# Optimization experiments

Hardware: AMD Instinct MI355X
Metric: run time of the kernel (lower is better)

Reference implementation:

```python
import jax, jax.numpy as jnp
import numpy as np

NUM_ANCHORS = 2
NUM_CLASSES = 20
H = 7
W = 7
IMG_H = 448
IMG_W = 448
NMS_THRESH = 0.7
SCORE_THRESH = 0.05
NBOX = H * W * NUM_ANCHORS  # 98 candidate boxes per image


def _format_outputs(x):
    # x: [b, H*W*(num_anchors*5 + num_classes)] -> decoded boxes/objectness/scores
    b = x.shape[0]
    x = x.reshape(b, H, W, NUM_ANCHORS * 5 + NUM_CLASSES)
    # class scores shared across anchors of a cell (repeat_interleave in torch)
    b_scores = jnp.broadcast_to(
        x[..., -NUM_CLASSES:].reshape(b, H * W, 1, NUM_CLASSES),
        (b, H * W, NUM_ANCHORS, NUM_CLASSES),
    )
    xa = x[..., : NUM_ANCHORS * 5].reshape(b, H, W, NUM_ANCHORS, 5)
    c_x = jnp.arange(W, dtype=x.dtype) * (IMG_W / W)
    c_y = jnp.arange(H, dtype=x.dtype) * (IMG_H / H)
    b_x = jax.nn.sigmoid(xa[..., 0]) + c_x[None, None, :, None]
    b_y = jax.nn.sigmoid(xa[..., 1]) + c_y[None, :, None, None]
    b_w = jax.nn.sigmoid(xa[..., 2])
    b_h = jax.nn.sigmoid(xa[..., 3])
    b_coords = jnp.stack((b_x, b_y, b_w, b_h), axis=-1).reshape(b, H * W, NUM_ANCHORS, 4)
    b_o = jax.nn.sigmoid(xa[..., 4]).reshape(b, H * W, NUM_ANCHORS)
    return b_coords, b_o, b_scores


def _pairwise_iou(boxes):
    # boxes: [n, 4] xyxy -> [n, n] IoU (torchvision box_iou semantics, 0 where union==0)
    area = (boxes[:, 2] - boxes[:, 0]) * (boxes[:, 3] - boxes[:, 1])
    lt = jnp.maximum(boxes[:, None, :2], boxes[None, :, :2])
    rb = jnp.minimum(boxes[:, None, 2:], boxes[None, :, 2:])
    wh = jnp.clip(rb - lt, 0.0)
    inter = wh[..., 0] * wh[..., 1]
    union = area[:, None] + area[None, :] - inter
    return jnp.where(union > 0, inter / union, 0.0)


def _per_image(coords, o, sc):
    # coords: [NBOX,4] (x,y,w,h), o: [NBOX], sc: [NBOX,NUM_CLASSES]
    valid = o >= 0.5  # objectness gate (b_o >= 0.5 selection in torch)
    labels = jnp.argmax(sc, axis=-1)
    scores = jnp.max(sc, axis=-1)
    # xywh -> xyxy, clamp to [0,1] (as in post_process)
    boxes = jnp.clip(
        jnp.concatenate([coords[:, :2], coords[:, :2] + coords[:, 2:]], axis=-1), 0.0, 1.0
    )
    # sort by score descending, invalid boxes pushed to the end
    s = jnp.where(valid, scores, -jnp.inf)
    order = jnp.argsort(-s)
    boxes_s = boxes[order]
    scores_s = scores[order]
    labels_s = labels[order]
    valid_s = valid[order]
    iou = _pairwise_iou(boxes_s)
    idxs = jnp.arange(NBOX)

    def body(i, alive):
        # if box i is still alive, suppress later boxes with IoU > thresh
        suppress = (iou[i] > NMS_THRESH) & (idxs > i) & alive[i]
        return alive & ~suppress

    alive = jax.lax.fori_loop(0, NBOX, body, valid_s)
    keep = alive & (scores_s >= SCORE_THRESH)
    boxes_out = jnp.where(keep[:, None], boxes_s, 0.0)
    scores_out = jnp.where(keep, scores_s, 0.0)
    labels_out = jnp.where(keep, labels_s, 0)
    return boxes_out, scores_out, labels_out, keep


def setup_inputs() -> dict:
    key = jax.random.key(0)
    x = jax.random.normal(key, (8192, H * W * (NUM_ANCHORS * 5 + NUM_CLASSES)), dtype=jnp.float32)
    return {"x": x}


def reference(x):
    b_coords, b_o, b_scores = _format_outputs(x)
    b = x.shape[0]
    coords = b_coords.reshape(b, -1, 4)
    o = b_o.reshape(b, -1)
    sc = b_scores.reshape(b, -1, NUM_CLASSES)
    boxes, scores, labels, keep = jax.vmap(_per_image)(coords, o, sc)
    # padded detections: [b, NBOX, 4], [b, NBOX], [b, NBOX], keep mask [b, NBOX]
    return boxes, scores, labels, keep
```

## Files before the change

kernel.cpp:

```cpp
#include <hip/hip_runtime.h>
#include <math.h>

#define NBOX 98
#define ROWLEN 1470
#define NMS_T 0.7f
#define SCORE_T 0.05f

__device__ __forceinline__ float sigm(float v) {
    return 1.0f / (1.0f + expf(-v));
}

__global__ __launch_bounds__(128) void yolo_post(const float* __restrict__ x,
                                                 float* __restrict__ out,
                                                 int batch) {
    const int b    = blockIdx.x;
    const int tid  = threadIdx.x;
    const int wid  = tid >> 6;
    const int lane = tid & 63;

    __shared__ float  row[ROWLEN];
    __shared__ float  cscore[NBOX];
    __shared__ float4 sbox[NBOX];
    __shared__ float  sarea[NBOX];
    __shared__ float  ssc[NBOX];
    __shared__ int    slab[NBOX];
    __shared__ unsigned long long m0[NBOX], m1[NBOX];
    __shared__ unsigned long long aliveW[2];
    __shared__ int    sCnt[2];

    const float2* xr2 = reinterpret_cast<const float2*>(x + (size_t)b * ROWLEN);
    float2* row2 = reinterpret_cast<float2*>(row);
    for (int i = tid; i < ROWLEN / 2; i += 128) row2[i] = xr2[i];
    __syncthreads();

    float4 box = make_float4(0.f, 0.f, 0.f, 0.f);
    float  mx  = 0.f;
    int    ml  = 0;
    bool   valid = false;
    if (tid < NBOX) {
        const int k  = tid >> 1;
        const int a  = tid & 1;
        const int ci = k / 7;
        const int cj = k - ci * 7;
        const float* p = row + k * 30 + a * 5;
        const float bx = sigm(p[0]) + (float)cj * 64.0f;
        const float by = sigm(p[1]) + (float)ci * 64.0f;
        const float bw = sigm(p[2]);
        const float bh = sigm(p[3]);
        valid = (p[4] >= 0.0f);

        const float* c = row + k * 30 + 10;
        mx = c[0]; ml = 0;
        #pragma unroll
        for (int t = 1; t < 20; ++t) {
            float v = c[t];
            if (v > mx) { mx = v; ml = t; }
        }
        box.x = fminf(fmaxf(bx, 0.f), 1.f);
        box.y = fminf(fmaxf(by, 0.f), 1.f);
        box.z = fminf(fmaxf(bx + bw, 0.f), 1.f);
        box.w = fminf(fmaxf(by + bh, 0.f), 1.f);
    }

    const unsigned long long bal = __ballot(valid);
    if (lane == 0) sCnt[wid] = (int)__popcll(bal);
    __syncthreads();
    const int V = sCnt[0] + sCnt[1];
    const int c = (int)__popcll(bal & ((1ull << lane) - 1ull)) + (wid ? sCnt[0] : 0);
    if (valid) cscore[c] = mx;
    __syncthreads();

    if (valid) {
        int rank = 0;
        for (int j = 0; j < V; ++j) {
            const float kj = cscore[j];
            rank += (kj > mx) || ((kj == mx) && (j < c));
        }
        sbox[rank]  = box;
        sarea[rank] = (box.z - box.x) * (box.w - box.y);
        ssc[rank]   = mx;
        slab[rank]  = ml;
    }
    __syncthreads();

    if (tid < V) {
        const float4 bi = sbox[tid];
        const float  ai = sarea[tid];
        unsigned long long mm0 = 0ull, mm1 = 0ull;
        const int e0 = (V < 64) ? V : 64;
        unsigned long long bit = 1ull;
        for (int j = 0; j < e0; ++j, bit <<= 1) {
            const float4 bj = sbox[j];
            const float w = fmaxf(fminf(bi.z, bj.z) - fmaxf(bi.x, bj.x), 0.f);
            const float h = fmaxf(fminf(bi.w, bj.w) - fmaxf(bi.y, bj.y), 0.f);
            const float inter = w * h;
            const float uni = (ai + sarea[j]) - inter;
            if (uni > 0.f && inter > NMS_T * uni) mm0 |= bit;
        }
        if (V > 64) {
            bit = 1ull;
            for (int j = 64; j < V; ++j, bit <<= 1) {
                const float4 bj = sbox[j];
                const float w = fmaxf(fminf(bi.z, bj.z) - fmaxf(bi.x, bj.x), 0.f);
                const float h = fmaxf(fminf(bi.w, bj.w) - fmaxf(bi.y, bj.y), 0.f);
                const float inter = w * h;
                const float uni = (ai + sarea[j]) - inter;
                if (uni > 0.f && inter > NMS_T * uni) mm1 |= bit;
            }
        }
        if (tid < 64) {
            mm0 &= ~((2ull << tid) - 1ull);
        } else {
            mm0 = 0ull;
            mm1 &= ~((2ull << (tid - 64)) - 1ull);
        }
        m0[tid] = mm0;
        m1[tid] = mm1;
    }
    __syncthreads();

    if (tid == 0) {
        if (V <= 64) {
            unsigned long long a0 = (V == 64) ? ~0ull : ((1ull << V) - 1ull);
            for (int i = 0; i < V; ++i)
                if ((a0 >> i) & 1ull) a0 &= ~m0[i];
            aliveW[0] = a0; aliveW[1] = 0ull;
        } else {
            unsigned long long a0 = ~0ull;
            unsigned long long a1 = (1ull << (V - 64)) - 1ull;
            for (int i = 0; i < 64; ++i)
                if ((a0 >> i) & 1ull) { a0 &= ~m0[i]; a1 &= ~m1[i]; }
            for (int i = 64; i < V; ++i)
                if ((a1 >> (i - 64)) & 1ull) a1 &= ~m1[i];
            aliveW[0] = a0; aliveW[1] = a1;
        }
    }
    __syncthreads();

    if (tid < NBOX) {
        float4 bo = make_float4(0.f, 0.f, 0.f, 0.f);
        float so = 0.f, lo = 0.f, ko = 0.f;
        if (tid < V) {
            const bool al = (tid < 64) ? ((aliveW[0] >> tid) & 1ull)
                                       : ((aliveW[1] >> (tid - 64)) & 1ull);
            const float s = ssc[tid];
            if (al && s >= SCORE_T) {
                bo = sbox[tid]; so = s; lo = (float)slab[tid]; ko = 1.0f;
            }
        }
        *reinterpret_cast<float4*>(out + (size_t)b * (NBOX * 4) + (size_t)tid * 4) = bo;
        const size_t base1 = (size_t)batch * (NBOX * 4);
        const size_t bn    = (size_t)batch * NBOX;
        out[base1 +          (size_t)b * NBOX + tid] = so;
        out[base1 + bn +     (size_t)b * NBOX + tid] = lo;
        out[base1 + 2 * bn + (size_t)b * NBOX + tid] = ko;
    }
}

extern "C" void kernel_launch(void* const* d_in, const int* in_sizes, int n_in,
                              void* d_out, int out_size, void* d_ws, size_t ws_size,
                              hipStream_t stream) {
    const float* x = (const float*)d_in[0];
    float* out = (float*)d_out;
    const int batch = in_sizes[0] / ROWLEN;
    yolo_post<<<batch, 128, 0, stream>>>(x, out, batch);
}
```

Baseline: 118.2 us.

## Split IoU mask work across both waves and alias shared buffers

The pairwise IoU matrix is now split by column half across the two waves. Previously wave 1 sat mostly idle while wave 0's threads looped over all V boxes. Each wave writes a partial suppression mask that is ORed during a now-branchless serial NMS scan. The shared-memory arrays for the sorted boxes, scores, areas and labels now alias the input row buffer to shrink LDS use, and the row load loop is unrolled. The trade-offs are doubled mask storage, extra OR work in the serial scan, and reliance on barrier ordering to keep the aliasing safe.

```diff
diff --git a/kernel.cpp b/kernel.cpp
--- a/kernel.cpp
+++ b/kernel.cpp
@@ -18,24 +18,29 @@
     const int wid  = tid >> 6;
     const int lane = tid & 63;
 
-    __shared__ float  row[ROWLEN];
-    __shared__ float  cscore[NBOX];
-    __shared__ float4 sbox[NBOX];
-    __shared__ float  sarea[NBOX];
-    __shared__ float  ssc[NBOX];
-    __shared__ int    slab[NBOX];
-    __shared__ unsigned long long m0[NBOX], m1[NBOX];
+    __shared__ __align__(16) char ubuf[ROWLEN * 4];
+    __shared__ unsigned long long m0h[2 * NBOX], m1h[2 * NBOX];
     __shared__ unsigned long long aliveW[2];
-    __shared__ int    sCnt[2];
+    __shared__ int sCnt[2];
+
+    float*  row    = reinterpret_cast<float*>(ubuf);
+    float4* sbox   = reinterpret_cast<float4*>(ubuf);
+    float*  cscore = reinterpret_cast<float*>(ubuf + 1568);
+    float*  sarea  = reinterpret_cast<float*>(ubuf + 1960);
+    float*  ssc    = reinterpret_cast<float*>(ubuf + 2352);
+    float*  slabf  = reinterpret_cast<float*>(ubuf + 2744);
 
     const float2* xr2 = reinterpret_cast<const float2*>(x + (size_t)b * ROWLEN);
     float2* row2 = reinterpret_cast<float2*>(row);
-    for (int i = tid; i < ROWLEN / 2; i += 128) row2[i] = xr2[i];
+    #pragma unroll
+    for (int i = 0; i < 6; ++i) {
+        const int idx = tid + i * 128;
+        if (idx < ROWLEN / 2) row2[idx] = xr2[idx];
+    }
     __syncthreads();
 
     float4 box = make_float4(0.f, 0.f, 0.f, 0.f);
-    float  mx  = 0.f;
-    int    ml  = 0;
+    float  mx  = 0.f, mlf = 0.f;
     bool   valid = false;
     if (tid < NBOX) {
         const int k  = tid >> 1;
@@ -49,13 +54,14 @@
         const float bh = sigm(p[3]);
         valid = (p[4] >= 0.0f);
 
-        const float* c = row + k * 30 + 10;
-        mx = c[0]; ml = 0;
+        const float* cc = row + k * 30 + 10;
+        mx = cc[0]; int ml = 0;
         #pragma unroll
         for (int t = 1; t < 20; ++t) {
-            float v = c[t];
+            const float v = cc[t];
             if (v > mx) { mx = v; ml = t; }
         }
+        mlf = (float)ml;
         box.x = fminf(fmaxf(bx, 0.f), 1.f);
         box.y = fminf(fmaxf(by, 0.f), 1.f);
         box.z = fminf(fmaxf(bx + bw, 0.f), 1.f);
@@ -79,61 +85,67 @@
         sbox[rank]  = box;
         sarea[rank] = (box.z - box.x) * (box.w - box.y);
         ssc[rank]   = mx;
-        slab[rank]  = ml;
+        slabf[rank] = mlf;
     }
     __syncthreads();
 
-    if (tid < V) {
-        const float4 bi = sbox[tid];
-        const float  ai = sarea[tid];
+    const int Vh  = (V + 1) >> 1;
+    const int jlo = wid ? Vh : 0;
+    const int jhi = wid ? V  : Vh;
+
+    auto iou_row = [&](int i) {
+        const float4 bi = sbox[i];
+        const float  ai = sarea[i];
         unsigned long long mm0 = 0ull, mm1 = 0ull;
-        const int e0 = (V < 64) ? V : 64;
-        unsigned long long bit = 1ull;
-        for (int j = 0; j < e0; ++j, bit <<= 1) {
+        const int e0 = (jhi < 64) ? jhi : 64;
+        for (int j = jlo; j < e0; ++j) {
             const float4 bj = sbox[j];
             const float w = fmaxf(fminf(bi.z, bj.z) - fmaxf(bi.x, bj.x), 0.f);
             const float h = fmaxf(fminf(bi.w, bj.w) - fmaxf(bi.y, bj.y), 0.f);
             const float inter = w * h;
             const float uni = (ai + sarea[j]) - inter;
-            if (uni > 0.f && inter > NMS_T * uni) mm0 |= bit;
+            if (uni > 0.f && inter > NMS_T * uni) mm0 |= (1ull << j);
         }
-        if (V > 64) {
-            bit = 1ull;
-            for (int j = 64; j < V; ++j, bit <<= 1) {
-                const float4 bj = sbox[j];
-                const float w = fmaxf(fminf(bi.z, bj.z) - fmaxf(bi.x, bj.x), 0.f);
-                const float h = fmaxf(fminf(bi.w, bj.w) - fmaxf(bi.y, bj.y), 0.f);
-                const float inter = w * h;
-                const float uni = (ai + sarea[j]) - inter;
-                if (uni > 0.f && inter > NMS_T * uni) mm1 |= bit;
-            }
+        const int s1 = (jlo > 64) ? jlo : 64;
+        for (int j = s1; j < jhi; ++j) {
+            const float4 bj = sbox[j];
+            const float w = fmaxf(fminf(bi.z, bj.z) - fmaxf(bi.x, bj.x), 0.f);
+            const float h = fmaxf(fminf(bi.w, bj.w) - fmaxf(bi.y, bj.y), 0.f);
+            const float inter = w * h;
+            const float uni = (ai + sarea[j]) - inter;
+            if (uni > 0.f && inter > NMS_T * uni) mm1 |= (1ull << (j - 64));
         }
-        if (tid < 64) {
-            mm0 &= ~((2ull << tid) - 1ull);
+        if (i < 64) {
+            mm0 &= ~((2ull << i) - 1ull);
         } else {
             mm0 = 0ull;
-            mm1 &= ~((2ull << (tid - 64)) - 1ull);
+            mm1 &= ~((2ull << (i - 64)) - 1ull);
         }
-        m0[tid] = mm0;
-        m1[tid] = mm1;
+        m0h[wid * NBOX + i] = mm0;
+        m1h[wid * NBOX + i] = mm1;
+    };
+
+    if (lane < V) iou_row(lane);
+    if (V > 64) {
+        const int i1 = 64 + lane;
+        if (i1 < V) iou_row(i1);
     }
     __syncthreads();
 
     if (tid == 0) {
-        if (V <= 64) {
-            unsigned long long a0 = (V == 64) ? ~0ull : ((1ull << V) - 1ull);
-            for (int i = 0; i < V; ++i)
-                if ((a0 >> i) & 1ull) a0 &= ~m0[i];
-            aliveW[0] = a0; aliveW[1] = 0ull;
-        } else {
-            unsigned long long a0 = ~0ull;
-            unsigned long long a1 = (1ull << (V - 64)) - 1ull;
-            for (int i = 0; i < 64; ++i)
-                if ((a0 >> i) & 1ull) { a0 &= ~m0[i]; a1 &= ~m1[i]; }
-            for (int i = 64; i < V; ++i)
-                if ((a1 >> (i - 64)) & 1ull) a1 &= ~m1[i];
-            aliveW[0] = a0; aliveW[1] = a1;
+        unsigned long long a0 = (V >= 64) ? ~0ull : ((1ull << V) - 1ull);
+        unsigned long long a1 = (V > 64) ? ((1ull << (V - 64)) - 1ull) : 0ull;
+        const int e = (V < 64) ? V : 64;
+        for (int i = 0; i < e; ++i) {
+            const unsigned long long take = 0ull - ((a0 >> i) & 1ull);
+            a0 &= ~((m0h[i] | m0h[NBOX + i]) & take);
+            a1 &= ~((m1h[i] | m1h[NBOX + i]) & take);
         }
+        for (int i = 64; i < V; ++i) {
+            const unsigned long long take = 0ull - ((a1 >> (i - 64)) & 1ull);
+            a1 &= ~((m1h[i] | m1h[NBOX + i]) & take);
+        }
+        aliveW[0] = a0; aliveW[1] = a1;
     }
     __syncthreads();
 
@@ -145,7 +157,7 @@
                                        : ((aliveW[1] >> (tid - 64)) & 1ull);
             const float s = ssc[tid];
             if (al && s >= SCORE_T) {
-                bo = sbox[tid]; so = s; lo = (float)slab[tid]; ko = 1.0f;
+                bo = sbox[tid]; so = s; lo = slabf[tid]; ko = 1.0f;
             }
         }
         *reinterpret_cast<float4*>(out + (size_t)b * (NBOX * 4) + (size_t)tid * 4) = bo;
```

Result: slower. 125.0 us (+5.7%).
